# Kernel tuning notes

Measured on AMD Instinct MI355X. Metric: run time of the kernel, lower is better.

## Reference

```python
import jax, jax.numpy as jnp
import numpy as np

N_NODES = 100000
NFEAT, NHID, NCLASS = 128, 64, 40
N_EDGES = 1600000


def setup_inputs() -> dict:
    key = jax.random.key(0)
    k1, k2, k3, k4, k5, k6 = jax.random.split(key, 6)
    x = jax.random.normal(k1, (N_NODES, NFEAT), dtype=jnp.float32)
    edge_index = jax.random.randint(k2, (2, N_EDGES), 0, N_NODES, dtype=jnp.int64)
    s1 = 1.0 / np.sqrt(NFEAT)
    s2 = 1.0 / np.sqrt(NHID)
    W1 = jax.random.uniform(k3, (NFEAT, NHID), jnp.float32, -s1, s1)
    b1 = jax.random.uniform(k4, (NHID,), jnp.float32, -s1, s1)
    W2 = jax.random.uniform(k5, (NHID, NCLASS), jnp.float32, -s2, s2)
    b2 = jax.random.uniform(k6, (NCLASS,), jnp.float32, -s2, s2)
    return {"x": x, "edge_index": edge_index, "W1": W1, "b1": b1, "W2": W2, "b2": b2}


def _gcn_conv(x, W, b, src, dst, n_nodes):
    # linear
    h = x @ W + b  # [N, out]
    # degree of source nodes (self-loops already included in src/dst)
    deg = jax.ops.segment_sum(jnp.ones_like(src, dtype=h.dtype), src, num_segments=n_nodes)
    dinv = deg ** -0.5  # deg >= 1 due to self-loops
    norm = dinv[src] * dinv[dst]  # [E]
    msg = norm[:, None] * h[src]  # gather + normalize, [E, out]
    return jax.ops.segment_sum(msg, dst, num_segments=n_nodes)  # scatter-add


def reference(x, edge_index, W1, b1, W2, b2):
    n = x.shape[0]
    loop = jnp.arange(n, dtype=edge_index.dtype)
    src = jnp.concatenate([edge_index[0], loop])
    dst = jnp.concatenate([edge_index[1], loop])
    h = _gcn_conv(x, W1, b1, src, dst, n)
    h = jax.nn.relu(h)
    # dropout is identity in eval mode
    h = _gcn_conv(h, W2, b2, src, dst, n)
    return jax.nn.log_softmax(h, axis=1)
```

## Files before the change

kernel.cpp:

```cpp
#include <hip/hip_runtime.h>
#include <hip/hip_fp8.h>
#include <math.h>

#define NFEAT 128
#define NHID 64
#define NCLASS 40
#define NCHUNK 64
#define RANGE_H 32768
#define RANGE_S 16384

typedef _Float16 half4_t __attribute__((ext_vector_type(4)));
typedef _Float16 half8_t __attribute__((ext_vector_type(8)));
typedef float f32x4 __attribute__((ext_vector_type(4)));

__device__ __forceinline__ float fp8f(unsigned b) {
    __hip_fp8_e4m3 h;
    h.__x = (__hip_fp8_storage_t)b;
    return (float)h;
}

__global__ __launch_bounds__(1024) void histdeg_kernel(
    const int* __restrict__ src, const int* __restrict__ dst, int E, int n,
    int nrange, unsigned short* __restrict__ deg_p,
    unsigned short* __restrict__ hist_p) {
    __shared__ unsigned int degc[RANGE_H / 2];
    __shared__ unsigned int histc[RANGE_H / 2];
    int c = blockIdx.x / nrange;
    int r = blockIdx.x - c * nrange;
    int r0 = r * RANGE_H;
    for (int i = threadIdx.x; i < RANGE_H / 2; i += 1024) {
        degc[i] = 0u;
        histc[i] = 0u;
    }
    __syncthreads();
    int e0 = (int)((long long)E * c / NCHUNK);
    int e1 = (int)((long long)E * (c + 1) / NCHUNK);
    for (int e = e0 + threadIdx.x * 4; e + 4 <= e1; e += 4096) {
        int4 s4 = *(const int4*)(src + e);
        int4 d4 = *(const int4*)(dst + e);
        int ss[4] = {s4.x, s4.y, s4.z, s4.w};
        int dd[4] = {d4.x, d4.y, d4.z, d4.w};
#pragma unroll
        for (int k = 0; k < 4; ++k) {
            int s = ss[k] - r0, d = dd[k] - r0;
            if ((unsigned)s < (unsigned)RANGE_H)
                atomicAdd(&degc[s >> 1], 1u << ((s & 1) * 16));
            if ((unsigned)d < (unsigned)RANGE_H)
                atomicAdd(&histc[d >> 1], 1u << ((d & 1) * 16));
        }
    }
    int tb = e0 + ((e1 - e0) & ~3);
    for (int e = tb + threadIdx.x; e < e1; e += 1024) {
        int s = src[e] - r0, d = dst[e] - r0;
        if ((unsigned)s < (unsigned)RANGE_H)
            atomicAdd(&degc[s >> 1], 1u << ((s & 1) * 16));
        if ((unsigned)d < (unsigned)RANGE_H)
            atomicAdd(&histc[d >> 1], 1u << ((d & 1) * 16));
    }
    __syncthreads();
    int hi = n - r0; if (hi > RANGE_H) hi = RANGE_H;
    for (int i = threadIdx.x; i < hi; i += 1024) {
        unsigned dv = (degc[i >> 1] >> ((i & 1) * 16)) & 0xFFFFu;
        unsigned hv = (histc[i >> 1] >> ((i & 1) * 16)) & 0xFFFFu;
        deg_p[(size_t)c * n + r0 + i] = (unsigned short)dv;
        hist_p[(size_t)c * n + r0 + i] = (unsigned short)hv;
    }
}

__global__ void reduce_kernel(const unsigned short* __restrict__ deg_p,
                              const unsigned short* __restrict__ hist_p,
                              float* __restrict__ dinv,
                              int* __restrict__ htot, int n) {
    int i = blockIdx.x * blockDim.x + threadIdx.x;
    if (i >= n) return;
    int d = 1, h = 0;
#pragma unroll 8
    for (int c = 0; c < NCHUNK; ++c) {
        d += deg_p[(size_t)c * n + i];
        h += hist_p[(size_t)c * n + i];
    }
    dinv[i] = rsqrtf((float)d);
    htot[i] = h;
}

__global__ void scan_block_kernel(const int* __restrict__ hist,
                                  int* __restrict__ scanned,
                                  int* __restrict__ bsums, int n) {
    __shared__ int tmp[256];
    int i = blockIdx.x * 256 + threadIdx.x;
    int v = (i < n) ? hist[i] : 0;
    tmp[threadIdx.x] = v;
    __syncthreads();
#pragma unroll
    for (int off = 1; off < 256; off <<= 1) {
        int t = (threadIdx.x >= off) ? tmp[threadIdx.x - off] : 0;
        __syncthreads();
        tmp[threadIdx.x] += t;
        __syncthreads();
    }
    if (i < n) scanned[i] = tmp[threadIdx.x] - v;
    if (threadIdx.x == 255) bsums[blockIdx.x] = tmp[255];
}

__global__ void scan_partials_kernel(int* __restrict__ bsums, int nb) {
    __shared__ int tmp[512];
    int v = (threadIdx.x < nb) ? bsums[threadIdx.x] : 0;
    tmp[threadIdx.x] = v;
    __syncthreads();
#pragma unroll
    for (int off = 1; off < 512; off <<= 1) {
        int t = (threadIdx.x >= off) ? tmp[threadIdx.x - off] : 0;
        __syncthreads();
        tmp[threadIdx.x] += t;
        __syncthreads();
    }
    if (threadIdx.x < nb) bsums[threadIdx.x] = tmp[threadIdx.x] - v;
}

__global__ void scan_add_kernel(const int* __restrict__ scanned,
                                const int* __restrict__ bsums,
                                int* __restrict__ row_start, int n, int E) {
    int i = blockIdx.x * 256 + threadIdx.x;
    if (i < n) row_start[i] = scanned[i] + bsums[blockIdx.x];
    if (i == 0) row_start[n] = E;
}

__global__ void base_kernel(const int* __restrict__ row_start,
                            const unsigned short* __restrict__ hist_p,
                            int* __restrict__ bases, int n) {
    int i = blockIdx.x * blockDim.x + threadIdx.x;
    if (i >= n) return;
    int r = row_start[i];
#pragma unroll 8
    for (int c = 0; c < NCHUNK; ++c) {
        bases[(size_t)c * n + i] = r;
        r += hist_p[(size_t)c * n + i];
    }
}

__global__ __launch_bounds__(1024) void scatter_kernel(
    const int* __restrict__ src, const int* __restrict__ dst, int E, int n,
    int nrange, const int* __restrict__ bases, int* __restrict__ es) {
    __shared__ int cur[RANGE_S];
    int c = blockIdx.x / nrange;
    int r = blockIdx.x - c * nrange;
    int r0 = r * RANGE_S;
    int hi = n - r0; if (hi > RANGE_S) hi = RANGE_S;
    for (int i = threadIdx.x; i < hi; i += 1024)
        cur[i] = bases[(size_t)c * n + r0 + i];
    __syncthreads();
    int e0 = (int)((long long)E * c / NCHUNK);
    int e1 = (int)((long long)E * (c + 1) / NCHUNK);
    for (int e = e0 + threadIdx.x * 4; e + 4 <= e1; e += 4096) {
        int4 s4 = *(const int4*)(src + e);
        int4 d4 = *(const int4*)(dst + e);
        int ss[4] = {s4.x, s4.y, s4.z, s4.w};
        int dd[4] = {d4.x, d4.y, d4.z, d4.w};
#pragma unroll
        for (int k = 0; k < 4; ++k) {
            int d = dd[k] - r0;
            if ((unsigned)d < (unsigned)hi) {
                int pos = atomicAdd(&cur[d], 1);
                es[pos] = ss[k];
            }
        }
    }
    int tb = e0 + ((e1 - e0) & ~3);
    for (int e = tb + threadIdx.x; e < e1; e += 1024) {
        int d = dst[e] - r0;
        if ((unsigned)d < (unsigned)hi) {
            int pos = atomicAdd(&cur[d], 1);
            es[pos] = src[e];
        }
    }
}

__global__ __launch_bounds__(256) void gemm1_mfma_kernel(
    const float* __restrict__ x, const float* __restrict__ W1,
    const float* __restrict__ b1, const float* __restrict__ dinv,
    unsigned char* __restrict__ H1f8, int n) {
    int wave = threadIdx.x >> 6;
    int lane = threadIdx.x & 63;
    int lr = lane & 15;
    int kg = lane >> 4;
    half8_t bf[4][4];
    float b1v[4];
#pragma unroll
    for (int t = 0; t < 4; ++t) {
        int col = t * 16 + lr;
        b1v[t] = b1[col];
#pragma unroll
        for (int ks = 0; ks < 4; ++ks) {
            int kb = ks * 32 + kg * 8;
            half8_t hb;
#pragma unroll
            for (int j = 0; j < 8; ++j) hb[j] = (_Float16)W1[(kb + j) * NHID + col];
            bf[ks][t] = hb;
        }
    }
    int nt16 = (n + 15) >> 4;
    for (int gt = blockIdx.x * 4 + wave; gt < nt16; gt += gridDim.x * 4) {
        int m0 = gt * 16;
        int arow = m0 + lr; if (arow >= n) arow = n - 1;
        f32x4 acc[4] = {f32x4{0,0,0,0}, f32x4{0,0,0,0}, f32x4{0,0,0,0}, f32x4{0,0,0,0}};
#pragma unroll
        for (int ks = 0; ks < 4; ++ks) {
            const float* ap = x + (size_t)arow * NFEAT + ks * 32 + kg * 8;
            float4 a0 = *(const float4*)ap;
            float4 a1 = *(const float4*)(ap + 4);
            half8_t af;
            af[0] = (_Float16)a0.x; af[1] = (_Float16)a0.y;
            af[2] = (_Float16)a0.z; af[3] = (_Float16)a0.w;
            af[4] = (_Float16)a1.x; af[5] = (_Float16)a1.y;
            af[6] = (_Float16)a1.z; af[7] = (_Float16)a1.w;
#pragma unroll
            for (int t = 0; t < 4; ++t)
                acc[t] = __builtin_amdgcn_mfma_f32_16x16x32_f16(af, bf[ks][t], acc[t], 0, 0, 0);
        }
        int r0 = m0 + kg * 4;
        float dv[4];
#pragma unroll
        for (int r = 0; r < 4; ++r) {
            int rr = r0 + r;
            dv[r] = (rr < n) ? dinv[rr] : 0.f;
        }
#pragma unroll
        for (int t = 0; t < 4; ++t)
#pragma unroll
            for (int r = 0; r < 4; ++r) {
                int rr = r0 + r;
                if (rr < n) {
                    __hip_fp8_e4m3 q((acc[t][r] + b1v[t]) * dv[r]);
                    H1f8[((size_t)rr << 6) + t * 16 + lr] = (unsigned char)q.__x;
                }
            }
    }
}

__global__ __launch_bounds__(256) void agg1_kernel(
    const int* __restrict__ es, const int* __restrict__ row_start,
    const float* __restrict__ dinv, const unsigned char* __restrict__ H1f8,
    _Float16* __restrict__ AGG, int n) {
    int wave = threadIdx.x >> 6;
    int lane = threadIdx.x & 63;
    int q = lane >> 4;
    int m = lane & 15;
    int stride = gridDim.x * 4;
    for (int node = blockIdx.x * 4 + wave; node < n; node += stride) {
        int e0 = row_start[node], e1 = row_start[node + 1];
        float a0 = 0.f, a1 = 0.f, a2 = 0.f, a3 = 0.f;
        for (int e = e0; e < e1; e += 64) {
            int cnt = e1 - e; if (cnt > 64) cnt = 64;
            int myE = es[e + ((lane < cnt) ? lane : 0)];
            for (int j = 0; j < cnt; j += 16) {
#pragma unroll
                for (int p = 0; p < 4; ++p) {
                    int jj = j + 4 * p + q;
                    int rr = __shfl(myE, jj, 64);
                    if (jj < cnt) {
                        unsigned w = *(const unsigned*)(H1f8 + ((size_t)rr << 6) + (m << 2));
                        a0 += fp8f(w & 0xFFu);
                        a1 += fp8f((w >> 8) & 0xFFu);
                        a2 += fp8f((w >> 16) & 0xFFu);
                        a3 += fp8f(w >> 24);
                    }
                }
            }
        }
        if (q == 0) {
            unsigned w = *(const unsigned*)(H1f8 + ((size_t)node << 6) + (m << 2));
            a0 += fp8f(w & 0xFFu);
            a1 += fp8f((w >> 8) & 0xFFu);
            a2 += fp8f((w >> 16) & 0xFFu);
            a3 += fp8f(w >> 24);
        }
        a0 += __shfl_xor(a0, 16, 64); a0 += __shfl_xor(a0, 32, 64);
        a1 += __shfl_xor(a1, 16, 64); a1 += __shfl_xor(a1, 32, 64);
        a2 += __shfl_xor(a2, 16, 64); a2 += __shfl_xor(a2, 32, 64);
        a3 += __shfl_xor(a3, 16, 64); a3 += __shfl_xor(a3, 32, 64);
        float di = dinv[node];
        if (lane < 16) {
            half4_t o;
            o[0] = (_Float16)fmaxf(a0 * di, 0.f);
            o[1] = (_Float16)fmaxf(a1 * di, 0.f);
            o[2] = (_Float16)fmaxf(a2 * di, 0.f);
            o[3] = (_Float16)fmaxf(a3 * di, 0.f);
            *(half4_t*)(AGG + ((size_t)node << 6) + (lane << 2)) = o;
        }
    }
}

__global__ __launch_bounds__(256) void gemm2_mfma_kernel(
    const _Float16* __restrict__ AGG, const float* __restrict__ W2,
    const float* __restrict__ b2, const float* __restrict__ dinv,
    _Float16* __restrict__ H2a, _Float16* __restrict__ H2b, int n) {
    int wave = threadIdx.x >> 6;
    int lane = threadIdx.x & 63;
    int lr = lane & 15;
    int kg = lane >> 4;
    half8_t bf[2][3];
    float b2v[3];
#pragma unroll
    for (int t = 0; t < 3; ++t) {
        int col = t * 16 + lr;
        b2v[t] = (col < NCLASS) ? b2[col] : 0.f;
#pragma unroll
        for (int ks = 0; ks < 2; ++ks) {
            int kb = ks * 32 + kg * 8;
            half8_t hb;
#pragma unroll
            for (int j = 0; j < 8; ++j)
                hb[j] = (col < NCLASS) ? (_Float16)W2[(kb + j) * NCLASS + col]
                                       : (_Float16)0.f;
            bf[ks][t] = hb;
        }
    }
    int nt16 = (n + 15) >> 4;
    for (int gt = blockIdx.x * 4 + wave; gt < nt16; gt += gridDim.x * 4) {
        int m0 = gt * 16;
        int arow = m0 + lr; if (arow >= n) arow = n - 1;
        f32x4 acc[3] = {f32x4{0,0,0,0}, f32x4{0,0,0,0}, f32x4{0,0,0,0}};
#pragma unroll
        for (int ks = 0; ks < 2; ++ks) {
            half8_t af = *(const half8_t*)(AGG + ((size_t)arow << 6) + ks * 32 + kg * 8);
#pragma unroll
            for (int t = 0; t < 3; ++t)
                acc[t] = __builtin_amdgcn_mfma_f32_16x16x32_f16(af, bf[ks][t], acc[t], 0, 0, 0);
        }
        int r0 = m0 + kg * 4;
        float dv[4];
#pragma unroll
        for (int r = 0; r < 4; ++r) {
            int rr = r0 + r;
            dv[r] = (rr < n) ? dinv[rr] : 0.f;
        }
#pragma unroll
        for (int t = 0; t < 3; ++t) {
            int col = t * 16 + lr;
#pragma unroll
            for (int r = 0; r < 4; ++r) {
                int rr = r0 + r;
                if (rr < n) {
                    _Float16 val = (_Float16)((acc[t][r] + b2v[t]) * dv[r]);
                    if (col < 32)
                        H2a[((size_t)rr << 5) + col] = val;
                    else if (col < NCLASS)
                        H2b[((size_t)rr << 3) + (col - 32)] = val;
                }
            }
        }
    }
}

__global__ __launch_bounds__(256) void agg2_lsm_kernel(
    const int* __restrict__ es, const int* __restrict__ row_start,
    const float* __restrict__ dinv, const _Float16* __restrict__ H2a,
    const _Float16* __restrict__ H2b, float* __restrict__ out, int n) {
    int wave = threadIdx.x >> 6;
    int lane = threadIdx.x & 63;
    int q = lane >> 4;
    int m = lane & 15;
    bool valid = (m < 10);
    int stride = gridDim.x * 4;
    for (int node = blockIdx.x * 4 + wave; node < n; node += stride) {
        int e0 = row_start[node], e1 = row_start[node + 1];
        half4_t acc4 = {(_Float16)0, (_Float16)0, (_Float16)0, (_Float16)0};
        for (int e = e0; e < e1; e += 64) {
            int cnt = e1 - e; if (cnt > 64) cnt = 64;
            int myE = es[e + ((lane < cnt) ? lane : 0)];
            for (int j = 0; j < cnt; j += 16) {
#pragma unroll
                for (int p = 0; p < 4; ++p) {
                    int jj = j + 4 * p + q;
                    int rr = __shfl(myE, jj, 64);
                    if (valid && jj < cnt) {
                        const _Float16* ptr = (m < 8)
                            ? H2a + (((size_t)rr << 5) + (m << 2))
                            : H2b + (((size_t)rr << 3) + ((m & 7) << 2));
                        acc4 += *(const half4_t*)ptr;
                    }
                }
            }
        }
        if (q == 0 && valid) {
            const _Float16* ptr = (m < 8)
                ? H2a + (((size_t)node << 5) + (m << 2))
                : H2b + (((size_t)node << 3) + ((m & 7) << 2));
            acc4 += *(const half4_t*)ptr;
        }
        union { half4_t h; int i[2]; } u, w;
        u.h = acc4;
        w.i[0] = __shfl_xor(u.i[0], 16, 64);
        w.i[1] = __shfl_xor(u.i[1], 16, 64);
        u.h += w.h;
        w.i[0] = __shfl_xor(u.i[0], 32, 64);
        w.i[1] = __shfl_xor(u.i[1], 32, 64);
        u.h += w.h;
        float di = dinv[node];
        float v0 = (float)u.h[0] * di, v1 = (float)u.h[1] * di;
        float v2 = (float)u.h[2] * di, v3 = (float)u.h[3] * di;
        float vmax = valid ? fmaxf(fmaxf(v0, v1), fmaxf(v2, v3)) : -INFINITY;
#pragma unroll
        for (int off = 8; off; off >>= 1) vmax = fmaxf(vmax, __shfl_xor(vmax, off, 64));
        float sume = valid ? (__expf(v0 - vmax) + __expf(v1 - vmax) +
                              __expf(v2 - vmax) + __expf(v3 - vmax)) : 0.f;
#pragma unroll
        for (int off = 8; off; off >>= 1) sume += __shfl_xor(sume, off, 64);
        float lse = __logf(sume) + vmax;
        if (lane < 10) {
            float4 o = make_float4(v0 - lse, v1 - lse, v2 - lse, v3 - lse);
            *(float4*)(out + (size_t)node * NCLASS + 4 * lane) = o;
        }
    }
}

extern "C" void kernel_launch(void* const* d_in, const int* in_sizes, int n_in,
                              void* d_out, int out_size, void* d_ws, size_t ws_size,
                              hipStream_t stream) {
    const float* x  = (const float*)d_in[0];
    const int*   ei = (const int*)d_in[1];
    const float* W1 = (const float*)d_in[2];
    const float* b1 = (const float*)d_in[3];
    const float* W2 = (const float*)d_in[4];
    const float* b2 = (const float*)d_in[5];
    float* out = (float*)d_out;

    const int n = in_sizes[0] / NFEAT;
    const int E = in_sizes[1] / 2;
    const int* src = ei;
    const int* dst = ei + E;
    const int nrange_h = (n + RANGE_H - 1) / RANGE_H;
    const int nrange_s = (n + RANGE_S - 1) / RANGE_S;

    char* ws = (char*)d_ws;
    float*          dinv      = (float*)(ws + 0);
    int*            htot      = (int*)(ws + (512 << 10));
    int*            scanned   = (int*)(ws + (1024 << 10));
    int*            row_start = (int*)(ws + (1536 << 10));
    int*            bsums     = (int*)(ws + (2048 << 10));
    unsigned short* deg_p     = (unsigned short*)(ws + (3u << 20));
    unsigned short* hist_p    = (unsigned short*)(ws + (16u << 20));
    int*            bases     = (int*)(ws + (29u << 20));
    int*            es        = (int*)(ws + (3u << 20));
    unsigned char*  H1f8      = (unsigned char*)(ws + (16u << 20));
    _Float16*       H2a       = (_Float16*)(ws + (23u << 20));
    _Float16*       H2b      = (_Float16*)(ws + (30u << 20));
    _Float16*       AGG       = (_Float16*)(ws + (32u << 20));

    const int blk = 256;
    const int nblk_n = (n + blk - 1) / blk;

    histdeg_kernel<<<NCHUNK * nrange_h, 1024, 0, stream>>>(src, dst, E, n, nrange_h,
                                                           deg_p, hist_p);
    reduce_kernel<<<nblk_n, blk, 0, stream>>>(deg_p, hist_p, dinv, htot, n);

    scan_block_kernel<<<nblk_n, blk, 0, stream>>>(htot, scanned, bsums, n);
    scan_partials_kernel<<<1, 512, 0, stream>>>(bsums, nblk_n);
    scan_add_kernel<<<nblk_n, blk, 0, stream>>>(scanned, bsums, row_start, n, E);
    base_kernel<<<nblk_n, blk, 0, stream>>>(row_start, hist_p, bases, n);

    scatter_kernel<<<NCHUNK * nrange_s, 1024, 0, stream>>>(src, dst, E, n, nrange_s,
                                                           bases, es);

    gemm1_mfma_kernel<<<512, blk, 0, stream>>>(x, W1, b1, dinv, H1f8, n);

    agg1_kernel<<<4096, blk, 0, stream>>>(es, row_start, dinv, H1f8, AGG, n);

    gemm2_mfma_kernel<<<512, blk, 0, stream>>>(AGG, W2, b2, dinv, H2a, H2b, n);

    agg2_lsm_kernel<<<4096, blk, 0, stream>>>(es, row_start, dinv, H2a, H2b, out, n);
}
```

Measured before the change: 302.4 us.

## Assign one node per 16-lane group in aggregation and store layer-2 features as fp8

Both aggregation kernels now give each 16-lane group its own node, replacing one node per 64-lane wave, and drop the cross-group shuffle reductions. Neighbour loads are unrolled four at a time to keep more gathers in flight. The second-layer features are quantized to fp8 in a single 64-byte-stride buffer instead of two fp16 arrays, which halves gather bytes for agg2. This trades extra fp8 rounding error in the class logits for lower memory traffic, and load balance now depends on per-node degree within each group.

```diff
diff --git a/kernel.cpp b/kernel.cpp
--- a/kernel.cpp
+++ b/kernel.cpp
@@ -15,7 +15,7 @@
 
 __device__ __forceinline__ float fp8f(unsigned b) {
     __hip_fp8_e4m3 h;
-    h.__x = (__hip_fp8_storage_t)b;
+    h.__x = (__hip_fp8_storage_t)(b & 0xFFu);
     return (float)h;
 }
 
@@ -243,57 +243,54 @@
     _Float16* __restrict__ AGG, int n) {
     int wave = threadIdx.x >> 6;
     int lane = threadIdx.x & 63;
-    int q = lane >> 4;
+    int g = lane >> 4;
     int m = lane & 15;
-    int stride = gridDim.x * 4;
-    for (int node = blockIdx.x * 4 + wave; node < n; node += stride) {
-        int e0 = row_start[node], e1 = row_start[node + 1];
-        float a0 = 0.f, a1 = 0.f, a2 = 0.f, a3 = 0.f;
-        for (int e = e0; e < e1; e += 64) {
-            int cnt = e1 - e; if (cnt > 64) cnt = 64;
-            int myE = es[e + ((lane < cnt) ? lane : 0)];
-            for (int j = 0; j < cnt; j += 16) {
-#pragma unroll
-                for (int p = 0; p < 4; ++p) {
-                    int jj = j + 4 * p + q;
-                    int rr = __shfl(myE, jj, 64);
-                    if (jj < cnt) {
-                        unsigned w = *(const unsigned*)(H1f8 + ((size_t)rr << 6) + (m << 2));
-                        a0 += fp8f(w & 0xFFu);
-                        a1 += fp8f((w >> 8) & 0xFFu);
-                        a2 += fp8f((w >> 16) & 0xFFu);
-                        a3 += fp8f(w >> 24);
-                    }
-                }
-            }
-        }
-        if (q == 0) {
-            unsigned w = *(const unsigned*)(H1f8 + ((size_t)node << 6) + (m << 2));
-            a0 += fp8f(w & 0xFFu);
-            a1 += fp8f((w >> 8) & 0xFFu);
-            a2 += fp8f((w >> 16) & 0xFFu);
-            a3 += fp8f(w >> 24);
-        }
-        a0 += __shfl_xor(a0, 16, 64); a0 += __shfl_xor(a0, 32, 64);
-        a1 += __shfl_xor(a1, 16, 64); a1 += __shfl_xor(a1, 32, 64);
-        a2 += __shfl_xor(a2, 16, 64); a2 += __shfl_xor(a2, 32, 64);
-        a3 += __shfl_xor(a3, 16, 64); a3 += __shfl_xor(a3, 32, 64);
+    int stride = gridDim.x * 16;
+    for (int node = blockIdx.x * 16 + wave * 4 + g; node < n; node += stride) {
+        int e0 = row_start[node];
+        int cnt = row_start[node + 1] - e0;
+        unsigned w = *(const unsigned*)(H1f8 + ((size_t)node << 6) + (m << 2));
+        float a0 = fp8f(w), a1 = fp8f(w >> 8), a2 = fp8f(w >> 16), a3 = fp8f(w >> 24);
+        for (int j = 0; j < cnt; j += 16) {
+            int rem = cnt - j;
+            int chunk = rem < 16 ? rem : 16;
+            int myE = es[e0 + j + ((m < rem) ? m : 0)];
+            int jj = 0;
+            for (; jj + 4 <= chunk; jj += 4) {
+                int r0 = __shfl(myE, (g << 4) + jj, 64);
+                int r1 = __shfl(myE, (g << 4) + jj + 1, 64);
+                int r2 = __shfl(myE, (g << 4) + jj + 2, 64);
+                int r3 = __shfl(myE, (g << 4) + jj + 3, 64);
+                unsigned w0 = *(const unsigned*)(H1f8 + ((size_t)r0 << 6) + (m << 2));
+                unsigned w1 = *(const unsigned*)(H1f8 + ((size_t)r1 << 6) + (m << 2));
+                unsigned w2 = *(const unsigned*)(H1f8 + ((size_t)r2 << 6) + (m << 2));
+                unsigned w3 = *(const unsigned*)(H1f8 + ((size_t)r3 << 6) + (m << 2));
+                a0 += fp8f(w0) + fp8f(w1) + fp8f(w2) + fp8f(w3);
+                a1 += fp8f(w0 >> 8) + fp8f(w1 >> 8) + fp8f(w2 >> 8) + fp8f(w3 >> 8);
+                a2 += fp8f(w0 >> 16) + fp8f(w1 >> 16) + fp8f(w2 >> 16) + fp8f(w3 >> 16);
+                a3 += fp8f(w0 >> 24) + fp8f(w1 >> 24) + fp8f(w2 >> 24) + fp8f(w3 >> 24);
+            }
+            for (; jj < chunk; ++jj) {
+                int rr = __shfl(myE, (g << 4) + jj, 64);
+                unsigned ww = *(const unsigned*)(H1f8 + ((size_t)rr << 6) + (m << 2));
+                a0 += fp8f(ww); a1 += fp8f(ww >> 8);
+                a2 += fp8f(ww >> 16); a3 += fp8f(ww >> 24);
+            }
+        }
         float di = dinv[node];
-        if (lane < 16) {
-            half4_t o;
-            o[0] = (_Float16)fmaxf(a0 * di, 0.f);
-            o[1] = (_Float16)fmaxf(a1 * di, 0.f);
-            o[2] = (_Float16)fmaxf(a2 * di, 0.f);
-            o[3] = (_Float16)fmaxf(a3 * di, 0.f);
-            *(half4_t*)(AGG + ((size_t)node << 6) + (lane << 2)) = o;
-        }
+        half4_t o;
+        o[0] = (_Float16)fmaxf(a0 * di, 0.f);
+        o[1] = (_Float16)fmaxf(a1 * di, 0.f);
+        o[2] = (_Float16)fmaxf(a2 * di, 0.f);
+        o[3] = (_Float16)fmaxf(a3 * di, 0.f);
+        *(half4_t*)(AGG + ((size_t)node << 6) + (m << 2)) = o;
     }
 }
 
 __global__ __launch_bounds__(256) void gemm2_mfma_kernel(
     const _Float16* __restrict__ AGG, const float* __restrict__ W2,
     const float* __restrict__ b2, const float* __restrict__ dinv,
-    _Float16* __restrict__ H2a, _Float16* __restrict__ H2b, int n) {
+    unsigned char* __restrict__ H2f8, int n) {
     int wave = threadIdx.x >> 6;
     int lane = threadIdx.x & 63;
     int lr = lane & 15;
@@ -337,15 +334,14 @@
 #pragma unroll
         for (int t = 0; t < 3; ++t) {
             int col = t * 16 + lr;
-#pragma unroll
-            for (int r = 0; r < 4; ++r) {
-                int rr = r0 + r;
-                if (rr < n) {
-                    _Float16 val = (_Float16)((acc[t][r] + b2v[t]) * dv[r]);
-                    if (col < 32)
-                        H2a[((size_t)rr << 5) + col] = val;
-                    else if (col < NCLASS)
-                        H2b[((size_t)rr << 3) + (col - 32)] = val;
+            if (col < NCLASS) {
+#pragma unroll
+                for (int r = 0; r < 4; ++r) {
+                    int rr = r0 + r;
+                    if (rr < n) {
+                        __hip_fp8_e4m3 q((acc[t][r] + b2v[t]) * dv[r]);
+                        H2f8[((size_t)rr << 6) + col] = (unsigned char)q.__x;
+                    }
                 }
             }
         }
@@ -354,51 +350,54 @@
 
 __global__ __launch_bounds__(256) void agg2_lsm_kernel(
     const int* __restrict__ es, const int* __restrict__ row_start,
-    const float* __restrict__ dinv, const _Float16* __restrict__ H2a,
-    const _Float16* __restrict__ H2b, float* __restrict__ out, int n) {
+    const float* __restrict__ dinv, const unsigned char* __restrict__ H2f8,
+    float* __restrict__ out, int n) {
     int wave = threadIdx.x >> 6;
     int lane = threadIdx.x & 63;
-    int q = lane >> 4;
+    int g = lane >> 4;
     int m = lane & 15;
     bool valid = (m < 10);
-    int stride = gridDim.x * 4;
-    for (int node = blockIdx.x * 4 + wave; node < n; node += stride) {
-        int e0 = row_start[node], e1 = row_start[node + 1];
-        half4_t acc4 = {(_Float16)0, (_Float16)0, (_Float16)0, (_Float16)0};
-        for (int e = e0; e < e1; e += 64) {
-            int cnt = e1 - e; if (cnt > 64) cnt = 64;
-            int myE = es[e + ((lane < cnt) ? lane : 0)];
-            for (int j = 0; j < cnt; j += 16) {
-#pragma unroll
-                for (int p = 0; p < 4; ++p) {
-                    int jj = j + 4 * p + q;
-                    int rr = __shfl(myE, jj, 64);
-                    if (valid && jj < cnt) {
-                        const _Float16* ptr = (m < 8)
-                            ? H2a + (((size_t)rr << 5) + (m << 2))
-                            : H2b + (((size_t)rr << 3) + ((m & 7) << 2));
-                        acc4 += *(const half4_t*)ptr;
-                    }
+    int stride = gridDim.x * 16;
+    for (int node = blockIdx.x * 16 + wave * 4 + g; node < n; node += stride) {
+        int e0 = row_start[node];
+        int cnt = row_start[node + 1] - e0;
+        float a0 = 0.f, a1 = 0.f, a2 = 0.f, a3 = 0.f;
+        if (valid) {
+            unsigned w = *(const unsigned*)(H2f8 + ((size_t)node << 6) + (m << 2));
+            a0 = fp8f(w); a1 = fp8f(w >> 8); a2 = fp8f(w >> 16); a3 = fp8f(w >> 24);
+        }
+        for (int j = 0; j < cnt; j += 16) {
+            int rem = cnt - j;
+            int chunk = rem < 16 ? rem : 16;
+            int myE = es[e0 + j + ((m < rem) ? m : 0)];
+            int jj = 0;
+            for (; jj + 4 <= chunk; jj += 4) {
+                int r0 = __shfl(myE, (g << 4) + jj, 64);
+                int r1 = __shfl(myE, (g << 4) + jj + 1, 64);
+                int r2 = __shfl(myE, (g << 4) + jj + 2, 64);
+                int r3 = __shfl(myE, (g << 4) + jj + 3, 64);
+                if (valid) {
+                    unsigned w0 = *(const unsigned*)(H2f8 + ((size_t)r0 << 6) + (m << 2));
+                    unsigned w1 = *(const unsigned*)(H2f8 + ((size_t)r1 << 6) + (m << 2));
+                    unsigned w2 = *(const unsigned*)(H2f8 + ((size_t)r2 << 6) + (m << 2));
+                    unsigned w3 = *(const unsigned*)(H2f8 + ((size_t)r3 << 6) + (m << 2));
+                    a0 += fp8f(w0) + fp8f(w1) + fp8f(w2) + fp8f(w3);
+                    a1 += fp8f(w0 >> 8) + fp8f(w1 >> 8) + fp8f(w2 >> 8) + fp8f(w3 >> 8);
+                    a2 += fp8f(w0 >> 16) + fp8f(w1 >> 16) + fp8f(w2 >> 16) + fp8f(w3 >> 16);
+                    a3 += fp8f(w0 >> 24) + fp8f(w1 >> 24) + fp8f(w2 >> 24) + fp8f(w3 >> 24);
                 }
             }
-        }
-        if (q == 0 && valid) {
-            const _Float16* ptr = (m < 8)
-                ? H2a + (((size_t)node << 5) + (m << 2))
-                : H2b + (((size_t)node << 3) + ((m & 7) << 2));
-            acc4 += *(const half4_t*)ptr;
-        }
-        union { half4_t h; int i[2]; } u, w;
-        u.h = acc4;
-        w.i[0] = __shfl_xor(u.i[0], 16, 64);
-        w.i[1] = __shfl_xor(u.i[1], 16, 64);
-        u.h += w.h;
-        w.i[0] = __shfl_xor(u.i[0], 32, 64);
-        w.i[1] = __shfl_xor(u.i[1], 32, 64);
-        u.h += w.h;
+            for (; jj < chunk; ++jj) {
+                int rr = __shfl(myE, (g << 4) + jj, 64);
+                if (valid) {
+                    unsigned ww = *(const unsigned*)(H2f8 + ((size_t)rr << 6) + (m << 2));
+                    a0 += fp8f(ww); a1 += fp8f(ww >> 8);
+                    a2 += fp8f(ww >> 16); a3 += fp8f(ww >> 24);
+                }
+            }
+        }
         float di = dinv[node];
-        float v0 = (float)u.h[0] * di, v1 = (float)u.h[1] * di;
-        float v2 = (float)u.h[2] * di, v3 = (float)u.h[3] * di;
+        float v0 = a0 * di, v1 = a1 * di, v2 = a2 * di, v3 = a3 * di;
         float vmax = valid ? fmaxf(fmaxf(v0, v1), fmaxf(v2, v3)) : -INFINITY;
 #pragma unroll
         for (int off = 8; off; off >>= 1) vmax = fmaxf(vmax, __shfl_xor(vmax, off, 64));
@@ -407,9 +406,9 @@
 #pragma unroll
         for (int off = 8; off; off >>= 1) sume += __shfl_xor(sume, off, 64);
         float lse = __logf(sume) + vmax;
-        if (lane < 10) {
+        if (valid) {
             float4 o = make_float4(v0 - lse, v1 - lse, v2 - lse, v3 - lse);
-            *(float4*)(out + (size_t)node * NCLASS + 4 * lane) = o;
+            *(float4*)(out + (size_t)node * NCLASS + (m << 2)) = o;
         }
     }
 }
@@ -443,8 +442,7 @@
     int*            bases     = (int*)(ws + (29u << 20));
     int*            es        = (int*)(ws + (3u << 20));
     unsigned char*  H1f8      = (unsigned char*)(ws + (16u << 20));
-    _Float16*       H2a       = (_Float16*)(ws + (23u << 20));
-    _Float16*       H2b      = (_Float16*)(ws + (30u << 20));
+    unsigned char*  H2f8      = (unsigned char*)(ws + (23u << 20));
     _Float16*       AGG       = (_Float16*)(ws + (32u << 20));
 
     const int blk = 256;
@@ -466,7 +464,7 @@
 
     agg1_kernel<<<4096, blk, 0, stream>>>(es, row_start, dinv, H1f8, AGG, n);
 
-    gemm2_mfma_kernel<<<512, blk, 0, stream>>>(AGG, W2, b2, dinv, H2a, H2b, n);
-
-    agg2_lsm_kernel<<<4096, blk, 0, stream>>>(es, row_start, dinv, H2a, H2b, out, n);
-}
+    gemm2_mfma_kernel<<<512, blk, 0, stream>>>(AGG, W2, b2, dinv, H2f8, n);
+
+    agg2_lsm_kernel<<<4096, blk, 0, stream>>>(es, row_start, dinv, H2f8, out, n);
+}
```

Result: faster. 261.6 us (-13.5%).
